# Kernel tuning notes

Measured on AMD Instinct MI355X. Metric: run time of the kernel, lower is better.

## Reference

```python
import jax, jax.numpy as jnp
import numpy as np

# Integration setup: torch code integrates t in [0,1] with dopri5.
# We use the dopri5 (RK45) Butcher tableau with a fixed step count so the
# reference is deterministic and jit/vjp friendly; per-stage math is identical.
N_STEPS = 16
T0, T1 = 0.0, 1.0

# dopri5 tableau
C2, C3, C4, C5, C6 = 1/5, 3/10, 4/5, 8/9, 1.0
A21 = 1/5
A31, A32 = 3/40, 9/40
A41, A42, A43 = 44/45, -56/15, 32/9
A51, A52, A53, A54 = 19372/6561, -25360/2187, 64448/6561, -212/729
A61, A62, A63, A64, A65 = 9017/3168, -355/33, 46732/5247, 49/176, -5103/18656
B1, B3, B4, B5, B6 = 35/384, 500/1113, 125/192, -2187/6784, 11/84  # 5th-order weights (b2=b7=0)


def setup_inputs() -> dict:
    key = jax.random.key(0)
    k0, k1, k2, k3 = jax.random.split(key, 4)
    B, D, H = 16384, 256, 512
    x = jax.random.normal(k0, (B, D), jnp.float32)
    W1 = jax.random.normal(k1, (D, H), jnp.float32) / np.sqrt(D).astype(np.float32)
    b1 = jnp.zeros((H,), jnp.float32)
    W2 = jax.random.normal(k2, (H, D), jnp.float32) / np.sqrt(H).astype(np.float32)
    b2 = jnp.zeros((D,), jnp.float32)
    Wfc = jax.random.normal(k3, (D, 1), jnp.float32) / np.sqrt(D).astype(np.float32)
    bfc = jnp.zeros((1,), jnp.float32)
    return {"x": x, "W1": W1, "b1": b1, "W2": W2, "b2": b2, "Wfc": Wfc, "bfc": bfc}


def reference(x, W1, b1, W2, b2, Wfc, bfc):
    def f(t, y):  # autonomous MLP vector field: dim -> hidden -> dim
        return jnp.tanh(y @ W1 + b1) @ W2 + b2

    dt = jnp.float32((T1 - T0) / N_STEPS)

    def step(carry, _):
        t, y = carry
        k1 = f(t, y)
        k2 = f(t + C2 * dt, y + dt * (A21 * k1))
        k3 = f(t + C3 * dt, y + dt * (A31 * k1 + A32 * k2))
        k4 = f(t + C4 * dt, y + dt * (A41 * k1 + A42 * k2 + A43 * k3))
        k5 = f(t + C5 * dt, y + dt * (A51 * k1 + A52 * k2 + A53 * k3 + A54 * k4))
        k6 = f(t + C6 * dt, y + dt * (A61 * k1 + A62 * k2 + A63 * k3 + A64 * k4 + A65 * k5))
        y_next = y + dt * (B1 * k1 + B3 * k3 + B4 * k4 + B5 * k5 + B6 * k6)
        return (t + dt, y_next), None

    (_, y1), _ = jax.lax.scan(step, (jnp.float32(T0), x), None, length=N_STEPS)
    return y1 @ Wfc + bfc  # [B, 1]
```

## Files before the change

kernel.cpp:

```cpp
#include <hip/hip_runtime.h>

typedef unsigned short u16;
typedef unsigned int   u32;
typedef __bf16 bf16x8 __attribute__((ext_vector_type(8)));
typedef float  f32x4  __attribute__((ext_vector_type(4)));
typedef u32    u32x2  __attribute__((ext_vector_type(2)));

#define DIMD  256
#define DIMH  512
#define MTILE 64
#define NTHREADS 512

#define USTR 264
#define HSTR 520
#define U_BASE 0
#define H_BASE (MTILE*USTR)
#define LDS_U16 (H_BASE + MTILE*HSTR)

#define DT 0.0625f

__device__ __forceinline__ u16 f2bf(float f) {
  u32 u = __float_as_uint(f);
  u += 0x7FFFu + ((u >> 16) & 1u);
  return (u16)(u >> 16);
}
__device__ __forceinline__ u32 pk(float a, float b) {
#if __has_builtin(__builtin_amdgcn_cvt_pk_bf16_f32)
  auto v = __builtin_amdgcn_cvt_pk_bf16_f32(a, b);
  u32 r; __builtin_memcpy(&r, &v, 4); return r;
#else
  return (u32)f2bf(a) | ((u32)f2bf(b) << 16);
#endif
}
__device__ __forceinline__ float bflo(u32 p) { return __uint_as_float(p << 16); }
__device__ __forceinline__ float bfhi(u32 p) { return __uint_as_float(p & 0xFFFF0000u); }
__device__ __forceinline__ float tanh_fast(float x) {
  float e = __builtin_amdgcn_exp2f(x * 2.8853900817779268f);
  return 1.0f - 2.0f * __builtin_amdgcn_rcpf(e + 1.0f);
}

__device__ __forceinline__ void bar_lds() {
  asm volatile("" ::: "memory");
  __builtin_amdgcn_s_waitcnt(0xC07F);
  __builtin_amdgcn_s_barrier();
  asm volatile("" ::: "memory");
}

__global__ void convert_w(const float* __restrict__ W1, const float* __restrict__ W2,
                          u16* __restrict__ w1t, u16* __restrict__ w2t) {
  int idx = blockIdx.x * 256 + threadIdx.x;
  {
    int n = idx >> 8, k = idx & 255;
    w1t[idx] = f2bf(W1[k * DIMH + n]);
  }
  {
    int n = idx >> 9, k = idx & 511;
    w2t[idx] = f2bf(W2[k * DIMD + n]);
  }
}

__device__ __forceinline__ void mfma_16(f32x4 (&acc)[4][4],
                                        const bf16x8 (&a)[4], const bf16x8 (&b)[4]) {
#pragma unroll
  for (int mb = 0; mb < 4; ++mb)
#pragma unroll
    for (int nb = 0; nb < 4; ++nb)
      acc[mb][nb] = __builtin_amdgcn_mfma_f32_16x16x32_bf16(a[mb], b[nb], acc[mb][nb], 0, 0, 0);
}
__device__ __forceinline__ void mfma_8(f32x4 (&acc)[2][4],
                                       const bf16x8 (&a)[2], const bf16x8 (&b)[4]) {
#pragma unroll
  for (int mb = 0; mb < 2; ++mb)
#pragma unroll
    for (int nb = 0; nb < 4; ++nb)
      acc[mb][nb] = __builtin_amdgcn_mfma_f32_16x16x32_bf16(a[mb], b[nb], acc[mb][nb], 0, 0, 0);
}

__global__ __attribute__((amdgpu_flat_work_group_size(NTHREADS, NTHREADS),
                          amdgpu_waves_per_eu(2, 2)))
void ode_fused(
    const float* __restrict__ x,   const float* __restrict__ b1,
    const float* __restrict__ b2,  const float* __restrict__ wfc,
    const float* __restrict__ bfc, const u16* __restrict__ w1t,
    const u16* __restrict__ w2t,   float* __restrict__ out)
{
  __shared__ u16 lds[LDS_U16];
  __shared__ u32 k2f[16 * NTHREADS];

  const int tid   = threadIdx.x;
  const int wg    = blockIdx.x;
  const int wv    = tid >> 6;
  const int lane  = tid & 63;
  const int lanel = lane & 15;
  const int laneq = lane >> 4;

  const u16* uRd = &lds[U_BASE + lanel * USTR + laneq * 8];
  const u16* hRd = &lds[H_BASE + lanel * HSTR + laneq * 8];
  u16* uWr = &lds[U_BASE + lanel * USTR + wv * 32 + laneq * 4];
  u16* hWr = &lds[H_BASE + lanel * HSTR + wv * 64 + laneq * 4];


  u32 b1p[8], b2p[4];
#pragma unroll
  for (int mb = 0; mb < 4; ++mb) {
    int base = wv * 64 + mb * 16 + laneq * 4;
    b1p[mb * 2 + 0] = pk(b1[base + 0], b1[base + 1]);
    b1p[mb * 2 + 1] = pk(b1[base + 2], b1[base + 3]);
  }
#pragma unroll
  for (int mb = 0; mb < 2; ++mb) {
    int base = wv * 32 + mb * 16 + laneq * 4;
    b2p[mb * 2 + 0] = pk(b2[base + 0], b2[base + 1]);
    b2p[mb * 2 + 1] = pk(b2[base + 2], b2[base + 3]);
  }

  float yv[32];
#pragma unroll
  for (int nb = 0; nb < 4; ++nb)
#pragma unroll
    for (int mb = 0; mb < 2; ++mb) {
      const float4 v = *(const float4*)&x[(wg * 64 + nb * 16 + lanel) * DIMD +
                                          wv * 32 + mb * 16 + laneq * 4];
      int i = nb * 8 + mb * 4;
      yv[i + 0] = v.x; yv[i + 1] = v.y; yv[i + 2] = v.z; yv[i + 3] = v.w;
    }

#pragma unroll
  for (int nb = 0; nb < 4; ++nb)
#pragma unroll
    for (int mb = 0; mb < 2; ++mb) {
      int i = nb * 8 + mb * 4;
      u32x2 w; w.x = pk(yv[i], yv[i + 1]); w.y = pk(yv[i + 2], yv[i + 3]);
      *(u32x2*)(uWr + nb * 16 * USTR + mb * 16) = w;
    }

  const u16* w1base[4];
#pragma unroll
  for (int mb = 0; mb < 4; ++mb)
    w1base[mb] = w1t + (wv * 64 + mb * 16 + lanel) * DIMD + laneq * 8;
  const u16* w2base[2];
#pragma unroll
  for (int mb = 0; mb < 2; ++mb)
    w2base[mb] = w2t + (wv * 32 + mb * 16 + lanel) * DIMH + laneq * 8;

  auto ldA1 = [&](bf16x8 (&a)[4], int kk) {
#pragma unroll
    for (int mb = 0; mb < 4; ++mb) a[mb] = *(const bf16x8*)(w1base[mb] + kk * 32);
  };
  auto ldB1 = [&](bf16x8 (&b)[4], int kk) {
#pragma unroll
    for (int nb = 0; nb < 4; ++nb) b[nb] = *(const bf16x8*)(uRd + nb * 16 * USTR + kk * 32);
  };
  auto ldA2 = [&](bf16x8 (&a)[2], int kk) {
#pragma unroll
    for (int mb = 0; mb < 2; ++mb) a[mb] = *(const bf16x8*)(w2base[mb] + kk * 32);
  };
  auto ldB2 = [&](bf16x8 (&b)[4], int kk) {
#pragma unroll
    for (int nb = 0; nb < 4; ++nb) b[nb] = *(const bf16x8*)(hRd + nb * 16 * HSTR + kk * 32);
  };

  u32 st[32];

  bf16x8 aP1[4];
  ldA1(aP1, 0);
  bar_lds();

#pragma unroll 1
  for (int step = 0; step < 16; ++step) {
#pragma unroll 1
    for (int s = 1; s <= 6; ++s) {
      f32x4 acc[4][4];
#pragma unroll
      for (int mb = 0; mb < 4; ++mb)
#pragma unroll
        for (int nb = 0; nb < 4; ++nb) acc[mb][nb] = (f32x4){0.f, 0.f, 0.f, 0.f};
      bf16x8 aA[4], bA[4], aB[4], bB[4];
#pragma unroll
      for (int mb = 0; mb < 4; ++mb) aA[mb] = aP1[mb];
      ldB1(bA, 0);
#pragma unroll 1
      for (int kk2 = 0; kk2 < 3; ++kk2) {
        ldA1(aB, 2 * kk2 + 1); ldB1(bB, 2 * kk2 + 1);
        mfma_16(acc, aA, bA);
        ldA1(aA, 2 * kk2 + 2); ldB1(bA, 2 * kk2 + 2);
        mfma_16(acc, aB, bB);
      }
      ldA1(aB, 7); ldB1(bB, 7);
      mfma_16(acc, aA, bA);
      bf16x8 aP2[2];
      ldA2(aP2, 0);
      mfma_16(acc, aB, bB);

#pragma unroll
      for (int mb = 0; mb < 4; ++mb)
#pragma unroll
        for (int nb = 0; nb < 4; ++nb) {
          float h0 = tanh_fast(acc[mb][nb][0] + bflo(b1p[mb * 2 + 0]));
          float h1 = tanh_fast(acc[mb][nb][1] + bfhi(b1p[mb * 2 + 0]));
          float h2 = tanh_fast(acc[mb][nb][2] + bflo(b1p[mb * 2 + 1]));
          float h3 = tanh_fast(acc[mb][nb][3] + bfhi(b1p[mb * 2 + 1]));
          u32x2 w; w.x = pk(h0, h1); w.y = pk(h2, h3);
          *(u32x2*)(hWr + nb * 16 * HSTR + mb * 16) = w;
        }
      bar_lds();

      f32x4 acc2[2][4];
#pragma unroll
      for (int mb = 0; mb < 2; ++mb)
#pragma unroll
        for (int nb = 0; nb < 4; ++nb) acc2[mb][nb] = (f32x4){0.f, 0.f, 0.f, 0.f};
      bf16x8 cA[2], dA[4], cB[2], dB[4];
#pragma unroll
      for (int mb = 0; mb < 2; ++mb) cA[mb] = aP2[mb];
      ldB2(dA, 0);
#pragma unroll 1
      for (int kk2 = 0; kk2 < 7; ++kk2) {
        ldA2(cB, 2 * kk2 + 1); ldB2(dB, 2 * kk2 + 1);
        mfma_8(acc2, cA, dA);
        ldA2(cA, 2 * kk2 + 2); ldB2(dA, 2 * kk2 + 2);
        mfma_8(acc2, cB, dB);
      }
      ldA2(cB, 15); ldB2(dB, 15);
      mfma_8(acc2, cA, dA);
      ldA1(aP1, 0);
      mfma_8(acc2, cB, dB);

      if (s == 1) {
        const float C = DT * 0.2f;
#pragma unroll
        for (int mb = 0; mb < 2; ++mb)
#pragma unroll
          for (int nb = 0; nb < 4; ++nb) {
            int i = nb * 8 + mb * 4, p = nb * 4 + mb * 2;
            float k0 = acc2[mb][nb][0] + bflo(b2p[mb * 2 + 0]);
            float k1 = acc2[mb][nb][1] + bfhi(b2p[mb * 2 + 0]);
            float k2 = acc2[mb][nb][2] + bflo(b2p[mb * 2 + 1]);
            float k3 = acc2[mb][nb][3] + bfhi(b2p[mb * 2 + 1]);
            st[p] = pk(k0, k1); st[p + 1] = pk(k2, k3);
            u32x2 w;
            w.x = pk(yv[i] + C * k0, yv[i + 1] + C * k1);
            w.y = pk(yv[i + 2] + C * k2, yv[i + 3] + C * k3);
            *(u32x2*)(uWr + nb * 16 * USTR + mb * 16) = w;
          }
      } else if (s == 2) {
        const float C1 = DT * 0.075f, C2 = DT * 0.225f;
#pragma unroll
        for (int mb = 0; mb < 2; ++mb)
#pragma unroll
          for (int nb = 0; nb < 4; ++nb) {
            int i = nb * 8 + mb * 4, p = nb * 4 + mb * 2;
            float k0 = acc2[mb][nb][0] + bflo(b2p[mb * 2 + 0]);
            float k1 = acc2[mb][nb][1] + bfhi(b2p[mb * 2 + 0]);
            float k2 = acc2[mb][nb][2] + bflo(b2p[mb * 2 + 1]);
            float k3 = acc2[mb][nb][3] + bfhi(b2p[mb * 2 + 1]);
            k2f[p * NTHREADS + tid]       = pk(k0, k1);
            k2f[(p + 1) * NTHREADS + tid] = pk(k2, k3);
            u32x2 w;
            w.x = pk(yv[i]     + C1 * bflo(st[p])     + C2 * k0,
                     yv[i + 1] + C1 * bfhi(st[p])     + C2 * k1);
            w.y = pk(yv[i + 2] + C1 * bflo(st[p + 1]) + C2 * k2,
                     yv[i + 3] + C1 * bfhi(st[p + 1]) + C2 * k3);
            *(u32x2*)(uWr + nb * 16 * USTR + mb * 16) = w;
          }
      } else if (s == 3) {
        const float C1 = DT * (float)(44.0/45.0);
        const float C2 = DT * (float)(-56.0/15.0);
        const float C3 = DT * (float)(32.0/9.0);
#pragma unroll
        for (int mb = 0; mb < 2; ++mb)
#pragma unroll
          for (int nb = 0; nb < 4; ++nb) {
            int i = nb * 8 + mb * 4, p = nb * 4 + mb * 2;
            float k0 = acc2[mb][nb][0] + bflo(b2p[mb * 2 + 0]);
            float k1 = acc2[mb][nb][1] + bfhi(b2p[mb * 2 + 0]);
            float k2 = acc2[mb][nb][2] + bflo(b2p[mb * 2 + 1]);
            float k3 = acc2[mb][nb][3] + bfhi(b2p[mb * 2 + 1]);
            st[16 + p] = pk(k0, k1); st[16 + p + 1] = pk(k2, k3);
            u32 q0 = k2f[p * NTHREADS + tid], q1 = k2f[(p + 1) * NTHREADS + tid];
            u32x2 w;
            w.x = pk(yv[i]     + C1 * bflo(st[p])     + C2 * bflo(q0) + C3 * k0,
                     yv[i + 1] + C1 * bfhi(st[p])     + C2 * bfhi(q0) + C3 * k1);
            w.y = pk(yv[i + 2] + C1 * bflo(st[p + 1]) + C2 * bflo(q1) + C3 * k2,
                     yv[i + 3] + C1 * bfhi(st[p + 1]) + C2 * bfhi(q1) + C3 * k3);
            *(u32x2*)(uWr + nb * 16 * USTR + mb * 16) = w;
          }
      } else if (s == 4) {
        const float C51 = DT * (float)(19372.0/6561.0);
        const float C52 = DT * (float)(-25360.0/2187.0);
        const float C53 = DT * (float)(64448.0/6561.0);
        const float C54 = DT * (float)(-212.0/729.0);
        const float D61 = DT * (float)(9017.0/3168.0  - 35.0/384.0);
        const float D62 = DT * (float)(-355.0/33.0);
        const float D63 = DT * (float)(46732.0/5247.0 - 500.0/1113.0);
        const float D64 = DT * (float)(49.0/176.0     - 125.0/192.0);
        const float E1  = DT * (float)(35.0/384.0);
        const float E3  = DT * (float)(500.0/1113.0);
        const float E4  = DT * (float)(125.0/192.0);
#pragma unroll
        for (int mb = 0; mb < 2; ++mb)
#pragma unroll
          for (int nb = 0; nb < 4; ++nb) {
            int i = nb * 8 + mb * 4, p = nb * 4 + mb * 2;
            float k40 = acc2[mb][nb][0] + bflo(b2p[mb * 2 + 0]);
            float k41 = acc2[mb][nb][1] + bfhi(b2p[mb * 2 + 0]);
            float k42 = acc2[mb][nb][2] + bflo(b2p[mb * 2 + 1]);
            float k43 = acc2[mb][nb][3] + bfhi(b2p[mb * 2 + 1]);
            float k10 = bflo(st[p]),      k11 = bfhi(st[p]);
            float k12 = bflo(st[p + 1]),  k13 = bfhi(st[p + 1]);
            u32 q0 = k2f[p * NTHREADS + tid], q1 = k2f[(p + 1) * NTHREADS + tid];
            float k20 = bflo(q0), k21 = bfhi(q0);
            float k22 = bflo(q1), k23 = bfhi(q1);
            float k30 = bflo(st[16 + p]),     k31 = bfhi(st[16 + p]);
            float k32 = bflo(st[16 + p + 1]), k33 = bfhi(st[16 + p + 1]);
            u32x2 w;
            w.x = pk(yv[i]     + C51 * k10 + C52 * k20 + C53 * k30 + C54 * k40,
                     yv[i + 1] + C51 * k11 + C52 * k21 + C53 * k31 + C54 * k41);
            w.y = pk(yv[i + 2] + C51 * k12 + C52 * k22 + C53 * k32 + C54 * k42,
                     yv[i + 3] + C51 * k13 + C52 * k23 + C53 * k33 + C54 * k43);
            *(u32x2*)(uWr + nb * 16 * USTR + mb * 16) = w;
            st[p]     = pk(D61 * k10 + D62 * k20 + D63 * k30 + D64 * k40,
                           D61 * k11 + D62 * k21 + D63 * k31 + D64 * k41);
            st[p + 1] = pk(D61 * k12 + D62 * k22 + D63 * k32 + D64 * k42,
                           D61 * k13 + D62 * k23 + D63 * k33 + D64 * k43);
            yv[i]     += E1 * k10 + E3 * k30 + E4 * k40;
            yv[i + 1] += E1 * k11 + E3 * k31 + E4 * k41;
            yv[i + 2] += E1 * k12 + E3 * k32 + E4 * k42;
            yv[i + 3] += E1 * k13 + E3 * k33 + E4 * k43;
          }
      } else if (s == 5) {
        const float D65 = DT * (float)(-5103.0/18656.0 + 2187.0/6784.0);
        const float E5  = DT * (float)(-2187.0/6784.0);
#pragma unroll
        for (int mb = 0; mb < 2; ++mb)
#pragma unroll
          for (int nb = 0; nb < 4; ++nb) {
            int i = nb * 8 + mb * 4, p = nb * 4 + mb * 2;
            float k0 = acc2[mb][nb][0] + bflo(b2p[mb * 2 + 0]);
            float k1 = acc2[mb][nb][1] + bfhi(b2p[mb * 2 + 0]);
            float k2 = acc2[mb][nb][2] + bflo(b2p[mb * 2 + 1]);
            float k3 = acc2[mb][nb][3] + bfhi(b2p[mb * 2 + 1]);
            u32x2 w;
            w.x = pk(yv[i]     + bflo(st[p])     + D65 * k0,
                     yv[i + 1] + bfhi(st[p])     + D65 * k1);
            w.y = pk(yv[i + 2] + bflo(st[p + 1]) + D65 * k2,
                     yv[i + 3] + bfhi(st[p + 1]) + D65 * k3);
            *(u32x2*)(uWr + nb * 16 * USTR + mb * 16) = w;
            yv[i]     += E5 * k0;
            yv[i + 1] += E5 * k1;
            yv[i + 2] += E5 * k2;
            yv[i + 3] += E5 * k3;
          }
      } else {
        const float E6 = DT * (float)(11.0/84.0);
#pragma unroll
        for (int mb = 0; mb < 2; ++mb)
#pragma unroll
          for (int nb = 0; nb < 4; ++nb) {
            int i = nb * 8 + mb * 4;
            yv[i]     += E6 * (acc2[mb][nb][0] + bflo(b2p[mb * 2 + 0]));
            yv[i + 1] += E6 * (acc2[mb][nb][1] + bfhi(b2p[mb * 2 + 0]));
            yv[i + 2] += E6 * (acc2[mb][nb][2] + bflo(b2p[mb * 2 + 1]));
            yv[i + 3] += E6 * (acc2[mb][nb][3] + bfhi(b2p[mb * 2 + 1]));
            u32x2 w;
            w.x = pk(yv[i], yv[i + 1]); w.y = pk(yv[i + 2], yv[i + 3]);
            *(u32x2*)(uWr + nb * 16 * USTR + mb * 16) = w;
          }
      }
      bar_lds();
    }
  }

  {
    float wfcv[8];
#pragma unroll
    for (int mb = 0; mb < 2; ++mb)
#pragma unroll
      for (int r = 0; r < 4; ++r)
        wfcv[mb * 4 + r] = wfc[wv * 32 + mb * 16 + laneq * 4 + r];
    float* redf = (float*)lds;
    float pr[4];
#pragma unroll
    for (int nb = 0; nb < 4; ++nb) {
      float p = 0.f;
#pragma unroll
      for (int mb = 0; mb < 2; ++mb)
#pragma unroll
        for (int r = 0; r < 4; ++r)
          p += yv[nb * 8 + mb * 4 + r] * wfcv[mb * 4 + r];
      p += __shfl_xor(p, 16);
      p += __shfl_xor(p, 32);
      pr[nb] = p;
    }
    if (laneq == 0) {
#pragma unroll
      for (int nb = 0; nb < 4; ++nb)
        redf[(nb * 16 + lanel) * 8 + wv] = pr[nb];
    }
    __syncthreads();
    if (tid < 64) {
      float s = bfc[0];
#pragma unroll
      for (int w = 0; w < 8; ++w) s += redf[tid * 8 + w];
      out[wg * 64 + tid] = s;
    }
  }
}

extern "C" void kernel_launch(void* const* d_in, const int* in_sizes, int n_in,
                              void* d_out, int out_size, void* d_ws, size_t ws_size,
                              hipStream_t stream) {
  const float* x   = (const float*)d_in[0];
  const float* W1  = (const float*)d_in[1];
  const float* b1  = (const float*)d_in[2];
  const float* W2  = (const float*)d_in[3];
  const float* b2  = (const float*)d_in[4];
  const float* wfc = (const float*)d_in[5];
  const float* bfc = (const float*)d_in[6];
  float* out = (float*)d_out;

  u16* w1t = (u16*)d_ws;
  u16* w2t = w1t + DIMH * DIMD;

  hipLaunchKernelGGL(convert_w, dim3(512), dim3(256), 0, stream, W1, W2, w1t, w2t);
  hipLaunchKernelGGL(ode_fused, dim3(16384 / MTILE), dim3(NTHREADS), 0, stream,
                     x, b1, b2, wfc, bfc, w1t, w2t, out);
}
```

Measured before the change: 1.617 ms.

## Split work across 16 waves per block and keep k2 stage in registers

Doubles the workgroup to 1024 threads. Each wave now computes half of the hidden tile in GEMM1, and GEMM2 splits along the row dimension, halving per-wave accumulators and y state. The k2 stage values, which were spilled to a large LDS array, are now kept in spare register slots because the per-wave footprint shrinks. This is meant to raise occupancy and latency hiding (waves_per_eu 4) and free LDS, at the cost of more redundant weight loads per block and more waves contending at barriers.

```diff
diff --git a/kernel.cpp b/kernel.cpp
--- a/kernel.cpp
+++ b/kernel.cpp
@@ -9,7 +9,7 @@
 #define DIMD  256
 #define DIMH  512
 #define MTILE 64
-#define NTHREADS 512
+#define NTHREADS 1024
 
 #define USTR 264
 #define HSTR 520
@@ -59,25 +59,25 @@
   }
 }
 
-__device__ __forceinline__ void mfma_16(f32x4 (&acc)[4][4],
-                                        const bf16x8 (&a)[4], const bf16x8 (&b)[4]) {
-#pragma unroll
-  for (int mb = 0; mb < 4; ++mb)
+__device__ __forceinline__ void mfma_g1(f32x4 (&acc)[2][4],
+                                        const bf16x8 (&a)[2], const bf16x8 (&b)[4]) {
+#pragma unroll
+  for (int mb = 0; mb < 2; ++mb)
 #pragma unroll
     for (int nb = 0; nb < 4; ++nb)
       acc[mb][nb] = __builtin_amdgcn_mfma_f32_16x16x32_bf16(a[mb], b[nb], acc[mb][nb], 0, 0, 0);
 }
-__device__ __forceinline__ void mfma_8(f32x4 (&acc)[2][4],
-                                       const bf16x8 (&a)[2], const bf16x8 (&b)[4]) {
+__device__ __forceinline__ void mfma_g2(f32x4 (&acc)[2][2],
+                                        const bf16x8 (&a)[2], const bf16x8 (&b)[2]) {
 #pragma unroll
   for (int mb = 0; mb < 2; ++mb)
 #pragma unroll
-    for (int nb = 0; nb < 4; ++nb)
+    for (int nb = 0; nb < 2; ++nb)
       acc[mb][nb] = __builtin_amdgcn_mfma_f32_16x16x32_bf16(a[mb], b[nb], acc[mb][nb], 0, 0, 0);
 }
 
 __global__ __attribute__((amdgpu_flat_work_group_size(NTHREADS, NTHREADS),
-                          amdgpu_waves_per_eu(2, 2)))
+                          amdgpu_waves_per_eu(4, 4)))
 void ode_fused(
     const float* __restrict__ x,   const float* __restrict__ b1,
     const float* __restrict__ b2,  const float* __restrict__ wfc,
@@ -85,48 +85,49 @@
     const u16* __restrict__ w2t,   float* __restrict__ out)
 {
   __shared__ u16 lds[LDS_U16];
-  __shared__ u32 k2f[16 * NTHREADS];
 
   const int tid   = threadIdx.x;
   const int wg    = blockIdx.x;
   const int wv    = tid >> 6;
+  const int wh    = wv >> 3;
+  const int wl    = wv & 7;
   const int lane  = tid & 63;
   const int lanel = lane & 15;
   const int laneq = lane >> 4;
 
-  const u16* uRd = &lds[U_BASE + lanel * USTR + laneq * 8];
-  const u16* hRd = &lds[H_BASE + lanel * HSTR + laneq * 8];
-  u16* uWr = &lds[U_BASE + lanel * USTR + wv * 32 + laneq * 4];
-  u16* hWr = &lds[H_BASE + lanel * HSTR + wv * 64 + laneq * 4];
-
-
-  u32 b1p[8], b2p[4];
-#pragma unroll
-  for (int mb = 0; mb < 4; ++mb) {
-    int base = wv * 64 + mb * 16 + laneq * 4;
+
+  u32 b1p[4], b2p[4];
+#pragma unroll
+  for (int mb = 0; mb < 2; ++mb) {
+    int base = wv * 32 + mb * 16 + laneq * 4;
     b1p[mb * 2 + 0] = pk(b1[base + 0], b1[base + 1]);
     b1p[mb * 2 + 1] = pk(b1[base + 2], b1[base + 3]);
   }
 #pragma unroll
   for (int mb = 0; mb < 2; ++mb) {
-    int base = wv * 32 + mb * 16 + laneq * 4;
+    int base = wl * 32 + mb * 16 + laneq * 4;
     b2p[mb * 2 + 0] = pk(b2[base + 0], b2[base + 1]);
     b2p[mb * 2 + 1] = pk(b2[base + 2], b2[base + 3]);
   }
 
-  float yv[32];
-#pragma unroll
-  for (int nb = 0; nb < 4; ++nb)
+  const u16* uRd = &lds[U_BASE + lanel * USTR + laneq * 8];
+  const u16* hRd = &lds[H_BASE + (wh * 32 + lanel) * HSTR + laneq * 8];
+  u16* hWr = &lds[H_BASE + lanel * HSTR + wv * 32 + laneq * 4];
+  u16* uWr = &lds[U_BASE + (wh * 32 + lanel) * USTR + wl * 32 + laneq * 4];
+
+  float yv[16];
+#pragma unroll
+  for (int nb = 0; nb < 2; ++nb)
 #pragma unroll
     for (int mb = 0; mb < 2; ++mb) {
-      const float4 v = *(const float4*)&x[(wg * 64 + nb * 16 + lanel) * DIMD +
-                                          wv * 32 + mb * 16 + laneq * 4];
+      const float4 v = *(const float4*)&x[(wg * 64 + wh * 32 + nb * 16 + lanel) * DIMD +
+                                          wl * 32 + mb * 16 + laneq * 4];
       int i = nb * 8 + mb * 4;
       yv[i + 0] = v.x; yv[i + 1] = v.y; yv[i + 2] = v.z; yv[i + 3] = v.w;
     }
 
 #pragma unroll
-  for (int nb = 0; nb < 4; ++nb)
+  for (int nb = 0; nb < 2; ++nb)
 #pragma unroll
     for (int mb = 0; mb < 2; ++mb) {
       int i = nb * 8 + mb * 4;
@@ -134,18 +135,18 @@
       *(u32x2*)(uWr + nb * 16 * USTR + mb * 16) = w;
     }
 
-  const u16* w1base[4];
-#pragma unroll
-  for (int mb = 0; mb < 4; ++mb)
-    w1base[mb] = w1t + (wv * 64 + mb * 16 + lanel) * DIMD + laneq * 8;
+  const u16* w1base[2];
+#pragma unroll
+  for (int mb = 0; mb < 2; ++mb)
+    w1base[mb] = w1t + (wv * 32 + mb * 16 + lanel) * DIMD + laneq * 8;
   const u16* w2base[2];
 #pragma unroll
   for (int mb = 0; mb < 2; ++mb)
-    w2base[mb] = w2t + (wv * 32 + mb * 16 + lanel) * DIMH + laneq * 8;
-
-  auto ldA1 = [&](bf16x8 (&a)[4], int kk) {
-#pragma unroll
-    for (int mb = 0; mb < 4; ++mb) a[mb] = *(const bf16x8*)(w1base[mb] + kk * 32);
+    w2base[mb] = w2t + (wl * 32 + mb * 16 + lanel) * DIMH + laneq * 8;
+
+  auto ldA1 = [&](bf16x8 (&a)[2], int kk) {
+#pragma unroll
+    for (int mb = 0; mb < 2; ++mb) a[mb] = *(const bf16x8*)(w1base[mb] + kk * 32);
   };
   auto ldB1 = [&](bf16x8 (&b)[4], int kk) {
 #pragma unroll
@@ -155,14 +156,14 @@
 #pragma unroll
     for (int mb = 0; mb < 2; ++mb) a[mb] = *(const bf16x8*)(w2base[mb] + kk * 32);
   };
-  auto ldB2 = [&](bf16x8 (&b)[4], int kk) {
-#pragma unroll
-    for (int nb = 0; nb < 4; ++nb) b[nb] = *(const bf16x8*)(hRd + nb * 16 * HSTR + kk * 32);
+  auto ldB2 = [&](bf16x8 (&b)[2], int kk) {
+#pragma unroll
+    for (int nb = 0; nb < 2; ++nb) b[nb] = *(const bf16x8*)(hRd + nb * 16 * HSTR + kk * 32);
   };
 
-  u32 st[32];
-
-  bf16x8 aP1[4];
+  u32 st[24];
+
+  bf16x8 aP1[2];
   ldA1(aP1, 0);
   bar_lds();
 
@@ -170,30 +171,29 @@
   for (int step = 0; step < 16; ++step) {
 #pragma unroll 1
     for (int s = 1; s <= 6; ++s) {
-      f32x4 acc[4][4];
-#pragma unroll
-      for (int mb = 0; mb < 4; ++mb)
+      f32x4 acc[2][4];
+#pragma unroll
+      for (int mb = 0; mb < 2; ++mb)
 #pragma unroll
         for (int nb = 0; nb < 4; ++nb) acc[mb][nb] = (f32x4){0.f, 0.f, 0.f, 0.f};
-      bf16x8 aA[4], bA[4], aB[4], bB[4];
-#pragma unroll
-      for (int mb = 0; mb < 4; ++mb) aA[mb] = aP1[mb];
-      ldB1(bA, 0);
+      bf16x8 aA[2], aB[2], bb[4];
+#pragma unroll
+      for (int mb = 0; mb < 2; ++mb) aA[mb] = aP1[mb];
 #pragma unroll 1
       for (int kk2 = 0; kk2 < 3; ++kk2) {
-        ldA1(aB, 2 * kk2 + 1); ldB1(bB, 2 * kk2 + 1);
-        mfma_16(acc, aA, bA);
-        ldA1(aA, 2 * kk2 + 2); ldB1(bA, 2 * kk2 + 2);
-        mfma_16(acc, aB, bB);
+        ldA1(aB, 2 * kk2 + 1);
+        ldB1(bb, 2 * kk2);     mfma_g1(acc, aA, bb);
+        ldA1(aA, 2 * kk2 + 2);
+        ldB1(bb, 2 * kk2 + 1); mfma_g1(acc, aB, bb);
       }
-      ldA1(aB, 7); ldB1(bB, 7);
-      mfma_16(acc, aA, bA);
+      ldA1(aB, 7);
+      ldB1(bb, 6); mfma_g1(acc, aA, bb);
       bf16x8 aP2[2];
       ldA2(aP2, 0);
-      mfma_16(acc, aB, bB);
-
-#pragma unroll
-      for (int mb = 0; mb < 4; ++mb)
+      ldB1(bb, 7); mfma_g1(acc, aB, bb);
+
+#pragma unroll
+      for (int mb = 0; mb < 2; ++mb)
 #pragma unroll
         for (int nb = 0; nb < 4; ++nb) {
           float h0 = tanh_fast(acc[mb][nb][0] + bflo(b1p[mb * 2 + 0]));
@@ -205,33 +205,32 @@
         }
       bar_lds();
 
-      f32x4 acc2[2][4];
+      f32x4 acc2[2][2];
 #pragma unroll
       for (int mb = 0; mb < 2; ++mb)
 #pragma unroll
-        for (int nb = 0; nb < 4; ++nb) acc2[mb][nb] = (f32x4){0.f, 0.f, 0.f, 0.f};
-      bf16x8 cA[2], dA[4], cB[2], dB[4];
+        for (int nb = 0; nb < 2; ++nb) acc2[mb][nb] = (f32x4){0.f, 0.f, 0.f, 0.f};
+      bf16x8 cA[2], cB[2], db[2];
 #pragma unroll
       for (int mb = 0; mb < 2; ++mb) cA[mb] = aP2[mb];
-      ldB2(dA, 0);
 #pragma unroll 1
       for (int kk2 = 0; kk2 < 7; ++kk2) {
-        ldA2(cB, 2 * kk2 + 1); ldB2(dB, 2 * kk2 + 1);
-        mfma_8(acc2, cA, dA);
-        ldA2(cA, 2 * kk2 + 2); ldB2(dA, 2 * kk2 + 2);
-        mfma_8(acc2, cB, dB);
+        ldA2(cB, 2 * kk2 + 1);
+        ldB2(db, 2 * kk2);     mfma_g2(acc2, cA, db);
+        ldA2(cA, 2 * kk2 + 2);
+        ldB2(db, 2 * kk2 + 1); mfma_g2(acc2, cB, db);
       }
-      ldA2(cB, 15); ldB2(dB, 15);
-      mfma_8(acc2, cA, dA);
+      ldA2(cB, 15);
+      ldB2(db, 14); mfma_g2(acc2, cA, db);
       ldA1(aP1, 0);
-      mfma_8(acc2, cB, dB);
+      ldB2(db, 15); mfma_g2(acc2, cB, db);
 
       if (s == 1) {
         const float C = DT * 0.2f;
 #pragma unroll
         for (int mb = 0; mb < 2; ++mb)
 #pragma unroll
-          for (int nb = 0; nb < 4; ++nb) {
+          for (int nb = 0; nb < 2; ++nb) {
             int i = nb * 8 + mb * 4, p = nb * 4 + mb * 2;
             float k0 = acc2[mb][nb][0] + bflo(b2p[mb * 2 + 0]);
             float k1 = acc2[mb][nb][1] + bfhi(b2p[mb * 2 + 0]);
@@ -248,14 +247,13 @@
 #pragma unroll
         for (int mb = 0; mb < 2; ++mb)
 #pragma unroll
-          for (int nb = 0; nb < 4; ++nb) {
+          for (int nb = 0; nb < 2; ++nb) {
             int i = nb * 8 + mb * 4, p = nb * 4 + mb * 2;
             float k0 = acc2[mb][nb][0] + bflo(b2p[mb * 2 + 0]);
             float k1 = acc2[mb][nb][1] + bfhi(b2p[mb * 2 + 0]);
             float k2 = acc2[mb][nb][2] + bflo(b2p[mb * 2 + 1]);
             float k3 = acc2[mb][nb][3] + bfhi(b2p[mb * 2 + 1]);
-            k2f[p * NTHREADS + tid]       = pk(k0, k1);
-            k2f[(p + 1) * NTHREADS + tid] = pk(k2, k3);
+            st[8 + p] = pk(k0, k1); st[8 + p + 1] = pk(k2, k3);
             u32x2 w;
             w.x = pk(yv[i]     + C1 * bflo(st[p])     + C2 * k0,
                      yv[i + 1] + C1 * bfhi(st[p])     + C2 * k1);
@@ -270,19 +268,18 @@
 #pragma unroll
         for (int mb = 0; mb < 2; ++mb)
 #pragma unroll
-          for (int nb = 0; nb < 4; ++nb) {
+          for (int nb = 0; nb < 2; ++nb) {
             int i = nb * 8 + mb * 4, p = nb * 4 + mb * 2;
             float k0 = acc2[mb][nb][0] + bflo(b2p[mb * 2 + 0]);
             float k1 = acc2[mb][nb][1] + bfhi(b2p[mb * 2 + 0]);
             float k2 = acc2[mb][nb][2] + bflo(b2p[mb * 2 + 1]);
             float k3 = acc2[mb][nb][3] + bfhi(b2p[mb * 2 + 1]);
             st[16 + p] = pk(k0, k1); st[16 + p + 1] = pk(k2, k3);
-            u32 q0 = k2f[p * NTHREADS + tid], q1 = k2f[(p + 1) * NTHREADS + tid];
-            u32x2 w;
-            w.x = pk(yv[i]     + C1 * bflo(st[p])     + C2 * bflo(q0) + C3 * k0,
-                     yv[i + 1] + C1 * bfhi(st[p])     + C2 * bfhi(q0) + C3 * k1);
-            w.y = pk(yv[i + 2] + C1 * bflo(st[p + 1]) + C2 * bflo(q1) + C3 * k2,
-                     yv[i + 3] + C1 * bfhi(st[p + 1]) + C2 * bfhi(q1) + C3 * k3);
+            u32x2 w;
+            w.x = pk(yv[i]     + C1 * bflo(st[p])     + C2 * bflo(st[8 + p])     + C3 * k0,
+                     yv[i + 1] + C1 * bfhi(st[p])     + C2 * bfhi(st[8 + p])     + C3 * k1);
+            w.y = pk(yv[i + 2] + C1 * bflo(st[p + 1]) + C2 * bflo(st[8 + p + 1]) + C3 * k2,
+                     yv[i + 3] + C1 * bfhi(st[p + 1]) + C2 * bfhi(st[8 + p + 1]) + C3 * k3);
             *(u32x2*)(uWr + nb * 16 * USTR + mb * 16) = w;
           }
       } else if (s == 4) {
@@ -300,17 +297,16 @@
 #pragma unroll
         for (int mb = 0; mb < 2; ++mb)
 #pragma unroll
-          for (int nb = 0; nb < 4; ++nb) {
+          for (int nb = 0; nb < 2; ++nb) {
             int i = nb * 8 + mb * 4, p = nb * 4 + mb * 2;
             float k40 = acc2[mb][nb][0] + bflo(b2p[mb * 2 + 0]);
             float k41 = acc2[mb][nb][1] + bfhi(b2p[mb * 2 + 0]);
             float k42 = acc2[mb][nb][2] + bflo(b2p[mb * 2 + 1]);
             float k43 = acc2[mb][nb][3] + bfhi(b2p[mb * 2 + 1]);
-            float k10 = bflo(st[p]),      k11 = bfhi(st[p]);
-            float k12 = bflo(st[p + 1]),  k13 = bfhi(st[p + 1]);
-            u32 q0 = k2f[p * NTHREADS + tid], q1 = k2f[(p + 1) * NTHREADS + tid];
-            float k20 = bflo(q0), k21 = bfhi(q0);
-            float k22 = bflo(q1), k23 = bfhi(q1);
+            float k10 = bflo(st[p]),     k11 = bfhi(st[p]);
+            float k12 = bflo(st[p + 1]), k13 = bfhi(st[p + 1]);
+            float k20 = bflo(st[8 + p]),     k21 = bfhi(st[8 + p]);
+            float k22 = bflo(st[8 + p + 1]), k23 = bfhi(st[8 + p + 1]);
             float k30 = bflo(st[16 + p]),     k31 = bfhi(st[16 + p]);
             float k32 = bflo(st[16 + p + 1]), k33 = bfhi(st[16 + p + 1]);
             u32x2 w;
@@ -334,7 +330,7 @@
 #pragma unroll
         for (int mb = 0; mb < 2; ++mb)
 #pragma unroll
-          for (int nb = 0; nb < 4; ++nb) {
+          for (int nb = 0; nb < 2; ++nb) {
             int i = nb * 8 + mb * 4, p = nb * 4 + mb * 2;
             float k0 = acc2[mb][nb][0] + bflo(b2p[mb * 2 + 0]);
             float k1 = acc2[mb][nb][1] + bfhi(b2p[mb * 2 + 0]);
@@ -356,7 +352,7 @@
 #pragma unroll
         for (int mb = 0; mb < 2; ++mb)
 #pragma unroll
-          for (int nb = 0; nb < 4; ++nb) {
+          for (int nb = 0; nb < 2; ++nb) {
             int i = nb * 8 + mb * 4;
             yv[i]     += E6 * (acc2[mb][nb][0] + bflo(b2p[mb * 2 + 0]));
             yv[i + 1] += E6 * (acc2[mb][nb][1] + bfhi(b2p[mb * 2 + 0]));
@@ -377,11 +373,11 @@
     for (int mb = 0; mb < 2; ++mb)
 #pragma unroll
       for (int r = 0; r < 4; ++r)
-        wfcv[mb * 4 + r] = wfc[wv * 32 + mb * 16 + laneq * 4 + r];
+        wfcv[mb * 4 + r] = wfc[wl * 32 + mb * 16 + laneq * 4 + r];
     float* redf = (float*)lds;
-    float pr[4];
-#pragma unroll
-    for (int nb = 0; nb < 4; ++nb) {
+    float pr[2];
+#pragma unroll
+    for (int nb = 0; nb < 2; ++nb) {
       float p = 0.f;
 #pragma unroll
       for (int mb = 0; mb < 2; ++mb)
@@ -394,8 +390,8 @@
     }
     if (laneq == 0) {
 #pragma unroll
-      for (int nb = 0; nb < 4; ++nb)
-        redf[(nb * 16 + lanel) * 8 + wv] = pr[nb];
+      for (int nb = 0; nb < 2; ++nb)
+        redf[(wh * 32 + nb * 16 + lanel) * 8 + wl] = pr[nb];
     }
     __syncthreads();
     if (tid < 64) {
```

Measured after the change: 2.540 ms. +57.1%, slower.
